# Kernel optimization log

Hardware: AMD Instinct MI355X
Metric: run time of the kernel (lower is better)

Reference implementation:

```python
import jax, jax.numpy as jnp
import numpy as np

N_NODES = 100000
N_EDGES = 3200000
IN_F, OUT_F = 256, 128


def setup_inputs() -> dict:
    key = jax.random.key(0)
    k1, k2, k3, k4, k5 = jax.random.split(key, 5)
    features = jax.random.normal(k1, (N_NODES, IN_F), dtype=jnp.float32)
    # Xavier-uniform-like init for the weight
    limit = float(np.sqrt(6.0 / (IN_F + OUT_F)))
    weight = jax.random.uniform(k2, (IN_F, OUT_F), dtype=jnp.float32, minval=-limit, maxval=limit)
    edge_row = jnp.sort(jax.random.randint(k3, (N_EDGES,), 0, N_NODES, dtype=jnp.int32))
    edge_col = jax.random.randint(k4, (N_EDGES,), 0, N_NODES, dtype=jnp.int32)
    edge_val = jax.random.uniform(k5, (N_EDGES,), dtype=jnp.float32)
    return {
        "features": features,
        "weight": weight,
        "edge_row": edge_row,
        "edge_col": edge_col,
        "edge_val": edge_val,
        "active": 1,
    }


def reference(features, weight, edge_row, edge_col, edge_val, active):
    # Dense transform: [N, in] @ [in, out] -> [N, out]
    h = features @ weight
    if active:  # static Python flag, matches `active=True` torch path
        h = jnp.tanh(h)
    # spmm(adj, h): out[r] = sum_e val[e] * h[col[e]] for edges with row[e]==r
    msgs = edge_val[:, None] * h[edge_col]          # [E, out] gather + scale
    out = jax.ops.segment_sum(msgs, edge_row, num_segments=N_NODES)
    return out
```

## Files before the change

kernel.cpp:

```cpp
#include <hip/hip_runtime.h>
#include <hip/hip_bf16.h>

#define N_NODES 100000
#define N_EDGES 3200000
#define IN_F 256
#define OUT_F 128

typedef __attribute__((ext_vector_type(8))) short bf16x8;
typedef __attribute__((ext_vector_type(4))) float f32x4;

__device__ __forceinline__ unsigned short f2bf(float f) {
    unsigned int u = __float_as_uint(f);
    u += 0x7fffu + ((u >> 16) & 1u);
    return (unsigned short)(u >> 16);
}

__device__ __forceinline__ short cvt_bf16(float f) {
    __hip_bfloat16 b = (__hip_bfloat16)f;
    return *reinterpret_cast<short*>(&b);
}

__global__ void k_init(const float* __restrict__ W, unsigned short* __restrict__ Wt,
                       const int* __restrict__ erow, int* __restrict__ row_ptr) {
    int e = blockIdx.x * 256 + threadIdx.x;
    if (e < IN_F * OUT_F) {
        int k = e >> 7;
        int c = e & 127;
        Wt[c * IN_F + k] = f2bf(W[e]);
    }
    if (e >= N_EDGES) return;
    int r = erow[e];
    int rprev = (e == 0) ? -1 : erow[e - 1];
    for (int rr = rprev + 1; rr <= r; ++rr) row_ptr[rr] = e;
    if (e == N_EDGES - 1) {
        for (int rr = r + 1; rr <= N_NODES; ++rr) row_ptr[rr] = N_EDGES;
    }
}

__global__ __launch_bounds__(256) void k_gemm(const float* __restrict__ A,
                                              const unsigned short* __restrict__ Wt,
                                              signed char* __restrict__ H8,
                                              const int* __restrict__ activep) {
    const int tid  = threadIdx.x;
    const int lane = tid & 63;
    const int wid  = tid >> 6;
    const int wr   = wid >> 1;
    const int wc   = wid & 1;
    const int brow = blockIdx.x * 128;
    const int l15  = lane & 15;
    const int lk   = (lane >> 4) * 8;

    const float* ap[4];
    #pragma unroll
    for (int i = 0; i < 4; ++i) {
        int row = brow + wr * 64 + i * 16 + l15;
        if (row > N_NODES - 1) row = N_NODES - 1;
        ap[i] = A + (long)row * IN_F + lk;
    }
    const unsigned short* bp = Wt + (long)(wc * 64 + l15) * IN_F + lk;

    f32x4 acc[4][4] = {};

    float4 f0[4], f1[4];
    #pragma unroll
    for (int i = 0; i < 4; ++i) {
        f0[i] = *(const float4*)(ap[i]);
        f1[i] = *(const float4*)(ap[i] + 4);
    }

    for (int k0 = 0; k0 < IN_F; k0 += 32) {
        const int kn = k0 + 32;
        float4 n0[4], n1[4];
        if (kn < IN_F) {
            #pragma unroll
            for (int i = 0; i < 4; ++i) {
                n0[i] = *(const float4*)(ap[i] + kn);
                n1[i] = *(const float4*)(ap[i] + kn + 4);
            }
        }
        bf16x8 a[4];
        #pragma unroll
        for (int i = 0; i < 4; ++i) {
            bf16x8 v;
            v[0] = cvt_bf16(f0[i].x); v[1] = cvt_bf16(f0[i].y);
            v[2] = cvt_bf16(f0[i].z); v[3] = cvt_bf16(f0[i].w);
            v[4] = cvt_bf16(f1[i].x); v[5] = cvt_bf16(f1[i].y);
            v[6] = cvt_bf16(f1[i].z); v[7] = cvt_bf16(f1[i].w);
            a[i] = v;
        }
        bf16x8 b[4];
        #pragma unroll
        for (int n = 0; n < 4; ++n)
            b[n] = *(const bf16x8*)(bp + (long)n * 16 * IN_F + k0);

        #pragma unroll
        for (int i = 0; i < 4; ++i)
            #pragma unroll
            for (int n = 0; n < 4; ++n)
                acc[i][n] = __builtin_amdgcn_mfma_f32_16x16x32_bf16(a[i], b[n], acc[i][n], 0, 0, 0);

        if (kn < IN_F) {
            #pragma unroll
            for (int i = 0; i < 4; ++i) { f0[i] = n0[i]; f1[i] = n1[i]; }
        }
    }

    const int act = *activep;
    const float qs = act ? 127.0f : 16.0f;
    #pragma unroll
    for (int i = 0; i < 4; ++i) {
        #pragma unroll
        for (int n = 0; n < 4; ++n) {
            #pragma unroll
            for (int r = 0; r < 4; ++r) {
                int row = brow + wr * 64 + i * 16 + (lane >> 4) * 4 + r;
                int col = wc * 64 + n * 16 + l15;
                if (row < N_NODES) {
                    float v = acc[i][n][r];
                    if (act) {
                        float t = __expf(2.0f * v);
                        v = 1.0f - __fdividef(2.0f, t + 1.0f);
                    }
                    float q = v * qs;
                    q = fminf(fmaxf(q, -127.0f), 127.0f);
                    H8[(long)row * OUT_F + col] = (signed char)__float2int_rn(q);
                }
            }
        }
    }
}

__global__ __launch_bounds__(256) void k_spmm(const int* __restrict__ row_ptr,
                                              const int* __restrict__ ecol,
                                              const float* __restrict__ eval,
                                              const signed char* __restrict__ h8,
                                              const int* __restrict__ activep,
                                              float* __restrict__ out) {
    const int lane = threadIdx.x & 63;
    const int w    = threadIdx.x >> 6;
    const int r    = blockIdx.x * 4 + w;
    if (r >= N_NODES) return;

    const int q  = lane >> 4;
    const int l15 = lane & 15;

    const int s = __builtin_amdgcn_readfirstlane(row_ptr[r]);
    const int e = __builtin_amdgcn_readfirstlane(row_ptr[r + 1]);
    const int act = __builtin_amdgcn_readfirstlane(*activep);
    const float invs = act ? (1.0f / 127.0f) : (1.0f / 16.0f);

    const signed char* hq = h8 + l15 * 8;

    float f0 = 0.f, f1 = 0.f, f2 = 0.f, f3 = 0.f;
    float f4 = 0.f, f5 = 0.f, f6 = 0.f, f7 = 0.f;

    for (int j = s; j < e; j += 16) {
        int   cc[4];
        float vv[4];
        #pragma unroll
        for (int u = 0; u < 4; ++u) {
            const int want = j + u * 4 + q;
            const int idx  = min(want, e - 1);
            cc[u] = ecol[idx];
            vv[u] = (want < e) ? eval[idx] * invs : 0.f;
        }
        uint2 g[4];
        #pragma unroll
        for (int u = 0; u < 4; ++u)
            g[u] = *(const uint2*)(hq + (((unsigned)cc[u]) << 7));
        #pragma unroll
        for (int u = 0; u < 4; ++u) {
            const float v = vv[u];
            const unsigned x = g[u].x, y = g[u].y;
            f0 = fmaf(v, (float)((signed char)(x      )), f0);
            f1 = fmaf(v, (float)((signed char)(x >>  8)), f1);
            f2 = fmaf(v, (float)((signed char)(x >> 16)), f2);
            f3 = fmaf(v, (float)((int)x >> 24),           f3);
            f4 = fmaf(v, (float)((signed char)(y      )), f4);
            f5 = fmaf(v, (float)((signed char)(y >>  8)), f5);
            f6 = fmaf(v, (float)((signed char)(y >> 16)), f6);
            f7 = fmaf(v, (float)((int)y >> 24),           f7);
        }
    }

    #pragma unroll
    for (int mask = 16; mask <= 32; mask <<= 1) {
        f0 += __shfl_xor(f0, mask);
        f1 += __shfl_xor(f1, mask);
        f2 += __shfl_xor(f2, mask);
        f3 += __shfl_xor(f3, mask);
        f4 += __shfl_xor(f4, mask);
        f5 += __shfl_xor(f5, mask);
        f6 += __shfl_xor(f6, mask);
        f7 += __shfl_xor(f7, mask);
    }

    if (q == 0) {
        float* dst = out + (long)r * OUT_F + l15 * 8;
        float4 o0; o0.x = f0; o0.y = f1; o0.z = f2; o0.w = f3;
        float4 o1; o1.x = f4; o1.y = f5; o1.z = f6; o1.w = f7;
        *(float4*)dst       = o0;
        *(float4*)(dst + 4) = o1;
    }
}

extern "C" void kernel_launch(void* const* d_in, const int* in_sizes, int n_in,
                              void* d_out, int out_size, void* d_ws, size_t ws_size,
                              hipStream_t stream) {
    const float* features = (const float*)d_in[0];
    const float* weight   = (const float*)d_in[1];
    const int*   erow     = (const int*)d_in[2];
    const int*   ecol     = (const int*)d_in[3];
    const float* evalp    = (const float*)d_in[4];
    const int*   activep  = (const int*)d_in[5];
    float* out = (float*)d_out;

    char* ws = (char*)d_ws;
    signed char* H8    = (signed char*)ws;
    unsigned short* Wt = (unsigned short*)(ws + 12800000);
    int* row_ptr       = (int*)(ws + 12800000 + 65536);

    k_init  <<<(N_EDGES + 255) / 256, 256, 0, stream>>>(weight, Wt, erow, row_ptr);
    k_gemm  <<<(N_NODES + 127) / 128, 256, 0, stream>>>(features, Wt, H8, activep);
    k_spmm  <<<(N_NODES + 3) / 4, 256, 0, stream>>>(row_ptr, ecol, evalp,
                                                    H8, activep, out);
}
```

Baseline: 149.3 us.

## Use biased uint8 features with hardware byte converts and deeper gather unroll in SpMM

The GEMM epilogue now stores the quantized features as unsigned bytes offset by 128. The SpMM converts them with v_cvt_f32_ubyteN and subtracts 128 times the sum of edge weights at the end, which removes the sign-extension shifts. The gather loop now processes 32 edges per iteration, with eight inline-asm dwordx2 loads using a scalar base and a 32-bit offset, followed by an explicit waitcnt. The goal is more memory-level parallelism and fewer ALU ops per edge. The cost is more registers, a forced full wait on each iteration, and extra float rounding from the bias subtraction.

Measured after the change: 158.7 us. 6.3% more time.

```diff
diff --git a/kernel.cpp b/kernel.cpp
--- a/kernel.cpp
+++ b/kernel.cpp
@@ -8,6 +8,7 @@
 
 typedef __attribute__((ext_vector_type(8))) short bf16x8;
 typedef __attribute__((ext_vector_type(4))) float f32x4;
+typedef __attribute__((ext_vector_type(2))) unsigned int u32x2;
 
 __device__ __forceinline__ unsigned short f2bf(float f) {
     unsigned int u = __float_as_uint(f);
@@ -19,6 +20,18 @@
     __hip_bfloat16 b = (__hip_bfloat16)f;
     return *reinterpret_cast<short*>(&b);
 }
+
+#if __has_builtin(__builtin_amdgcn_cvt_f32_ubyte0)
+#define UB0(x) __builtin_amdgcn_cvt_f32_ubyte0(x)
+#define UB1(x) __builtin_amdgcn_cvt_f32_ubyte1(x)
+#define UB2(x) __builtin_amdgcn_cvt_f32_ubyte2(x)
+#define UB3(x) __builtin_amdgcn_cvt_f32_ubyte3(x)
+#else
+#define UB0(x) ((float)((unsigned char)((x))))
+#define UB1(x) ((float)((unsigned char)((x) >> 8)))
+#define UB2(x) ((float)((unsigned char)((x) >> 16)))
+#define UB3(x) ((float)((x) >> 24))
+#endif
 
 __global__ void k_init(const float* __restrict__ W, unsigned short* __restrict__ Wt,
                        const int* __restrict__ erow, int* __restrict__ row_ptr) {
@@ -39,7 +52,7 @@
 
 __global__ __launch_bounds__(256) void k_gemm(const float* __restrict__ A,
                                               const unsigned short* __restrict__ Wt,
-                                              signed char* __restrict__ H8,
+                                              unsigned char* __restrict__ H8,
                                               const int* __restrict__ activep) {
     const int tid  = threadIdx.x;
     const int lane = tid & 63;
@@ -123,7 +136,8 @@
                     }
                     float q = v * qs;
                     q = fminf(fmaxf(q, -127.0f), 127.0f);
-                    H8[(long)row * OUT_F + col] = (signed char)__float2int_rn(q);
+                    H8[(long)row * OUT_F + col] =
+                        (unsigned char)(__float2int_rn(q) + 128);
                 }
             }
         }
@@ -133,7 +147,7 @@
 __global__ __launch_bounds__(256) void k_spmm(const int* __restrict__ row_ptr,
                                               const int* __restrict__ ecol,
                                               const float* __restrict__ eval,
-                                              const signed char* __restrict__ h8,
+                                              const unsigned char* __restrict__ h8,
                                               const int* __restrict__ activep,
                                               float* __restrict__ out) {
     const int lane = threadIdx.x & 63;
@@ -141,47 +155,72 @@
     const int r    = blockIdx.x * 4 + w;
     if (r >= N_NODES) return;
 
-    const int q  = lane >> 4;
+    const int q   = lane >> 4;
     const int l15 = lane & 15;
+    const unsigned dqb = (unsigned)l15 * 8u;
 
     const int s = __builtin_amdgcn_readfirstlane(row_ptr[r]);
     const int e = __builtin_amdgcn_readfirstlane(row_ptr[r + 1]);
     const int act = __builtin_amdgcn_readfirstlane(*activep);
     const float invs = act ? (1.0f / 127.0f) : (1.0f / 16.0f);
 
-    const signed char* hq = h8 + l15 * 8;
-
     float f0 = 0.f, f1 = 0.f, f2 = 0.f, f3 = 0.f;
     float f4 = 0.f, f5 = 0.f, f6 = 0.f, f7 = 0.f;
-
-    for (int j = s; j < e; j += 16) {
-        int   cc[4];
-        float vv[4];
-        #pragma unroll
-        for (int u = 0; u < 4; ++u) {
+    float vs = 0.f;
+
+    for (int j = s; j < e; j += 32) {
+        int   cc[8];
+        float vv[8];
+        #pragma unroll
+        for (int u = 0; u < 8; ++u) {
             const int want = j + u * 4 + q;
             const int idx  = min(want, e - 1);
             cc[u] = ecol[idx];
             vv[u] = (want < e) ? eval[idx] * invs : 0.f;
         }
-        uint2 g[4];
-        #pragma unroll
-        for (int u = 0; u < 4; ++u)
-            g[u] = *(const uint2*)(hq + (((unsigned)cc[u]) << 7));
-        #pragma unroll
-        for (int u = 0; u < 4; ++u) {
-            const float v = vv[u];
-            const unsigned x = g[u].x, y = g[u].y;
-            f0 = fmaf(v, (float)((signed char)(x      )), f0);
-            f1 = fmaf(v, (float)((signed char)(x >>  8)), f1);
-            f2 = fmaf(v, (float)((signed char)(x >> 16)), f2);
-            f3 = fmaf(v, (float)((int)x >> 24),           f3);
-            f4 = fmaf(v, (float)((signed char)(y      )), f4);
-            f5 = fmaf(v, (float)((signed char)(y >>  8)), f5);
-            f6 = fmaf(v, (float)((signed char)(y >> 16)), f6);
-            f7 = fmaf(v, (float)((int)y >> 24),           f7);
-        }
-    }
+        const unsigned o0 = dqb + (((unsigned)cc[0]) << 7);
+        const unsigned o1 = dqb + (((unsigned)cc[1]) << 7);
+        const unsigned o2 = dqb + (((unsigned)cc[2]) << 7);
+        const unsigned o3 = dqb + (((unsigned)cc[3]) << 7);
+        const unsigned o4 = dqb + (((unsigned)cc[4]) << 7);
+        const unsigned o5 = dqb + (((unsigned)cc[5]) << 7);
+        const unsigned o6 = dqb + (((unsigned)cc[6]) << 7);
+        const unsigned o7 = dqb + (((unsigned)cc[7]) << 7);
+
+        u32x2 g0, g1, g2, g3, g4, g5, g6, g7;
+        asm volatile("global_load_dwordx2 %0, %1, %2" : "=v"(g0) : "v"(o0), "s"(h8));
+        asm volatile("global_load_dwordx2 %0, %1, %2" : "=v"(g1) : "v"(o1), "s"(h8));
+        asm volatile("global_load_dwordx2 %0, %1, %2" : "=v"(g2) : "v"(o2), "s"(h8));
+        asm volatile("global_load_dwordx2 %0, %1, %2" : "=v"(g3) : "v"(o3), "s"(h8));
+        asm volatile("global_load_dwordx2 %0, %1, %2" : "=v"(g4) : "v"(o4), "s"(h8));
+        asm volatile("global_load_dwordx2 %0, %1, %2" : "=v"(g5) : "v"(o5), "s"(h8));
+        asm volatile("global_load_dwordx2 %0, %1, %2" : "=v"(g6) : "v"(o6), "s"(h8));
+        asm volatile("global_load_dwordx2 %0, %1, %2" : "=v"(g7) : "v"(o7), "s"(h8));
+        asm volatile("s_waitcnt vmcnt(0)" ::: "memory");
+        __builtin_amdgcn_sched_barrier(0);
+
+        #define EDGE_FMA(G, V)                      \
+            do {                                    \
+                const float v_ = (V);               \
+                vs += v_;                           \
+                const unsigned x_ = (G).x, y_ = (G).y; \
+                f0 = fmaf(v_, UB0(x_), f0);         \
+                f1 = fmaf(v_, UB1(x_), f1);         \
+                f2 = fmaf(v_, UB2(x_), f2);         \
+                f3 = fmaf(v_, UB3(x_), f3);         \
+                f4 = fmaf(v_, UB0(y_), f4);         \
+                f5 = fmaf(v_, UB1(y_), f5);         \
+                f6 = fmaf(v_, UB2(y_), f6);         \
+                f7 = fmaf(v_, UB3(y_), f7);         \
+            } while (0)
+        EDGE_FMA(g0, vv[0]); EDGE_FMA(g1, vv[1]); EDGE_FMA(g2, vv[2]); EDGE_FMA(g3, vv[3]);
+        EDGE_FMA(g4, vv[4]); EDGE_FMA(g5, vv[5]); EDGE_FMA(g6, vv[6]); EDGE_FMA(g7, vv[7]);
+        #undef EDGE_FMA
+    }
+
+    const float bias = 128.0f * vs;
+    f0 -= bias; f1 -= bias; f2 -= bias; f3 -= bias;
+    f4 -= bias; f5 -= bias; f6 -= bias; f7 -= bias;
 
     #pragma unroll
     for (int mask = 16; mask <= 32; mask <<= 1) {
@@ -197,10 +236,10 @@
 
     if (q == 0) {
         float* dst = out + (long)r * OUT_F + l15 * 8;
-        float4 o0; o0.x = f0; o0.y = f1; o0.z = f2; o0.w = f3;
-        float4 o1; o1.x = f4; o1.y = f5; o1.z = f6; o1.w = f7;
-        *(float4*)dst       = o0;
-        *(float4*)(dst + 4) = o1;
+        float4 o0v; o0v.x = f0; o0v.y = f1; o0v.z = f2; o0v.w = f3;
+        float4 o1v; o1v.x = f4; o1v.y = f5; o1v.z = f6; o1v.w = f7;
+        *(float4*)dst       = o0v;
+        *(float4*)(dst + 4) = o1v;
     }
 }
 
@@ -216,7 +255,7 @@
     float* out = (float*)d_out;
 
     char* ws = (char*)d_ws;
-    signed char* H8    = (signed char*)ws;
+    unsigned char* H8  = (unsigned char*)ws;
     unsigned short* Wt = (unsigned short*)(ws + 12800000);
     int* row_ptr       = (int*)(ws + 12800000 + 65536);
 
```

## Software-pipeline SpMM gathers and switch to offset-unsigned int8 encoding

Applied to the files above, without the earlier changes.

The SpMM loop is restructured into a two-stage software pipeline: edge indices and values are loaded two iterations ahead and the feature-row gathers one iteration ahead, so memory latency overlaps with the FMAs. The int8 features are stored biased by +128 as unsigned bytes, which allows cheaper unsigned byte-to-float conversion; the bias is removed afterwards using the sum of edge weights. Empty rows now take an early exit that writes zeros. The bias subtraction can add float rounding error, and the prefetch raises register pressure.

New measurement: 173.4 us. +16.2%, slower.

```diff
diff --git a/kernel.cpp b/kernel.cpp
--- a/kernel.cpp
+++ b/kernel.cpp
@@ -19,6 +19,11 @@
     __hip_bfloat16 b = (__hip_bfloat16)f;
     return *reinterpret_cast<short*>(&b);
 }
+
+#define UB0(x) ((float)((unsigned char)((x))))
+#define UB1(x) ((float)((unsigned char)((x) >> 8)))
+#define UB2(x) ((float)((unsigned char)((x) >> 16)))
+#define UB3(x) ((float)((x) >> 24))
 
 __global__ void k_init(const float* __restrict__ W, unsigned short* __restrict__ Wt,
                        const int* __restrict__ erow, int* __restrict__ row_ptr) {
@@ -39,7 +44,7 @@
 
 __global__ __launch_bounds__(256) void k_gemm(const float* __restrict__ A,
                                               const unsigned short* __restrict__ Wt,
-                                              signed char* __restrict__ H8,
+                                              unsigned char* __restrict__ H8,
                                               const int* __restrict__ activep) {
     const int tid  = threadIdx.x;
     const int lane = tid & 63;
@@ -123,7 +128,8 @@
                     }
                     float q = v * qs;
                     q = fminf(fmaxf(q, -127.0f), 127.0f);
-                    H8[(long)row * OUT_F + col] = (signed char)__float2int_rn(q);
+                    H8[(long)row * OUT_F + col] =
+                        (unsigned char)(__float2int_rn(q) + 128);
                 }
             }
         }
@@ -133,7 +139,7 @@
 __global__ __launch_bounds__(256) void k_spmm(const int* __restrict__ row_ptr,
                                               const int* __restrict__ ecol,
                                               const float* __restrict__ eval,
-                                              const signed char* __restrict__ h8,
+                                              const unsigned char* __restrict__ h8,
                                               const int* __restrict__ activep,
                                               float* __restrict__ out) {
     const int lane = threadIdx.x & 63;
@@ -141,47 +147,100 @@
     const int r    = blockIdx.x * 4 + w;
     if (r >= N_NODES) return;
 
-    const int q  = lane >> 4;
+    const int q   = lane >> 4;
     const int l15 = lane & 15;
+    const unsigned dqb = (unsigned)l15 * 8u;
 
     const int s = __builtin_amdgcn_readfirstlane(row_ptr[r]);
     const int e = __builtin_amdgcn_readfirstlane(row_ptr[r + 1]);
+
+    if (s >= e) {
+        if (q == 0) {
+            float4 z = {0.f, 0.f, 0.f, 0.f};
+            float* dst = out + (long)r * OUT_F + l15 * 8;
+            *(float4*)dst       = z;
+            *(float4*)(dst + 4) = z;
+        }
+        return;
+    }
+
     const int act = __builtin_amdgcn_readfirstlane(*activep);
     const float invs = act ? (1.0f / 127.0f) : (1.0f / 16.0f);
-
-    const signed char* hq = h8 + l15 * 8;
+    const unsigned char* hq = h8 + dqb;
 
     float f0 = 0.f, f1 = 0.f, f2 = 0.f, f3 = 0.f;
     float f4 = 0.f, f5 = 0.f, f6 = 0.f, f7 = 0.f;
+    float vs = 0.f;
+
+    #define LDE(jj, CC, VV)                                         \
+        do {                                                        \
+            _Pragma("unroll")                                       \
+            for (int u = 0; u < 4; ++u) {                           \
+                const int want = (jj) + u * 4 + q;                  \
+                const int idx  = min(want, e - 1);                  \
+                CC[u] = ecol[idx];                                  \
+                VV[u] = (want < e) ? eval[idx] * invs : 0.f;        \
+            }                                                       \
+        } while (0)
+
+    #define GATHER(CC, G)                                           \
+        do {                                                        \
+            _Pragma("unroll")                                       \
+            for (int u = 0; u < 4; ++u)                             \
+                G[u] = *(const uint2*)(hq + (((unsigned)CC[u]) << 7)); \
+        } while (0)
+
+    #define FMA8(G, V)                                              \
+        do {                                                        \
+            _Pragma("unroll")                                       \
+            for (int u = 0; u < 4; ++u) {                           \
+                const float v_ = V[u];                              \
+                vs += v_;                                           \
+                const unsigned x_ = G[u].x, y_ = G[u].y;            \
+                f0 = fmaf(v_, UB0(x_), f0);                         \
+                f1 = fmaf(v_, UB1(x_), f1);                         \
+                f2 = fmaf(v_, UB2(x_), f2);                         \
+                f3 = fmaf(v_, UB3(x_), f3);                         \
+                f4 = fmaf(v_, UB0(y_), f4);                         \
+                f5 = fmaf(v_, UB1(y_), f5);                         \
+                f6 = fmaf(v_, UB2(y_), f6);                         \
+                f7 = fmaf(v_, UB3(y_), f7);                         \
+            }                                                       \
+        } while (0)
+
+    int   ccB[4];
+    float vvA[4], vvB[4];
+    uint2 gA[4];
+    {
+        int ccA[4];
+        LDE(s, ccA, vvA);
+        GATHER(ccA, gA);
+        LDE(s + 16, ccB, vvB);
+    }
 
     for (int j = s; j < e; j += 16) {
-        int   cc[4];
-        float vv[4];
+        uint2 gB[4];
+        GATHER(ccB, gB);
+        int   ccN[4];
+        float vvN[4];
+        LDE(j + 32, ccN, vvN);
+        FMA8(gA, vvA);
         #pragma unroll
         for (int u = 0; u < 4; ++u) {
-            const int want = j + u * 4 + q;
-            const int idx  = min(want, e - 1);
-            cc[u] = ecol[idx];
-            vv[u] = (want < e) ? eval[idx] * invs : 0.f;
-        }
-        uint2 g[4];
-        #pragma unroll
-        for (int u = 0; u < 4; ++u)
-            g[u] = *(const uint2*)(hq + (((unsigned)cc[u]) << 7));
-        #pragma unroll
-        for (int u = 0; u < 4; ++u) {
-            const float v = vv[u];
-            const unsigned x = g[u].x, y = g[u].y;
-            f0 = fmaf(v, (float)((signed char)(x      )), f0);
-            f1 = fmaf(v, (float)((signed char)(x >>  8)), f1);
-            f2 = fmaf(v, (float)((signed char)(x >> 16)), f2);
-            f3 = fmaf(v, (float)((int)x >> 24),           f3);
-            f4 = fmaf(v, (float)((signed char)(y      )), f4);
-            f5 = fmaf(v, (float)((signed char)(y >>  8)), f5);
-            f6 = fmaf(v, (float)((signed char)(y >> 16)), f6);
-            f7 = fmaf(v, (float)((int)y >> 24),           f7);
-        }
-    }
+            gA[u]  = gB[u];
+            ccB[u] = ccN[u];
+            vvA[u] = vvB[u];
+            vvB[u] = vvN[u];
+        }
+    }
+
+    #undef LDE
+    #undef GATHER
+    #undef FMA8
+
+    const float bias = 128.0f * vs;
+    f0 -= bias; f1 -= bias; f2 -= bias; f3 -= bias;
+    f4 -= bias; f5 -= bias; f6 -= bias; f7 -= bias;
 
     #pragma unroll
     for (int mask = 16; mask <= 32; mask <<= 1) {
@@ -197,10 +256,10 @@
 
     if (q == 0) {
         float* dst = out + (long)r * OUT_F + l15 * 8;
-        float4 o0; o0.x = f0; o0.y = f1; o0.z = f2; o0.w = f3;
-        float4 o1; o1.x = f4; o1.y = f5; o1.z = f6; o1.w = f7;
-        *(float4*)dst       = o0;
-        *(float4*)(dst + 4) = o1;
+        float4 o0v; o0v.x = f0; o0v.y = f1; o0v.z = f2; o0v.w = f3;
+        float4 o1v; o1v.x = f4; o1v.y = f5; o1v.z = f6; o1v.w = f7;
+        *(float4*)dst       = o0v;
+        *(float4*)(dst + 4) = o1v;
     }
 }
 
@@ -216,7 +275,7 @@
     float* out = (float*)d_out;
 
     char* ws = (char*)d_ws;
-    signed char* H8    = (signed char*)ws;
+    unsigned char* H8  = (unsigned char*)ws;
     unsigned short* Wt = (unsigned short*)(ws + 12800000);
     int* row_ptr       = (int*)(ws + 12800000 + 65536);
 
```

## Switch SpMM to edge-chunk partitioning with atomic row flushes

Applied to the files above, without the earlier changes.

Drops the row_ptr construction and row-per-wavefront SpMM. Instead, each 16-lane group processes a fixed chunk of 104 consecutive edges, reading row, col and val with vector loads, and accumulates runs of equal rows before flushing them to the output with atomicAdd. H is stored as offset-unsigned bytes, corrected by subtracting 128 times the summed weights, which allows cheaper byte-to-float conversion. Costs added: a memset of the output, float atomics on the output, and non-deterministic summation order.

New measurement: 546.7 us. +266.2%, slower.

```diff
diff --git a/kernel.cpp b/kernel.cpp
--- a/kernel.cpp
+++ b/kernel.cpp
@@ -6,6 +6,9 @@
 #define IN_F 256
 #define OUT_F 128
 
+#define CHUNK 104
+#define SPMM_BLOCKS 1924
+
 typedef __attribute__((ext_vector_type(8))) short bf16x8;
 typedef __attribute__((ext_vector_type(4))) float f32x4;
 
@@ -20,26 +23,22 @@
     return *reinterpret_cast<short*>(&b);
 }
 
-__global__ void k_init(const float* __restrict__ W, unsigned short* __restrict__ Wt,
-                       const int* __restrict__ erow, int* __restrict__ row_ptr) {
-    int e = blockIdx.x * 256 + threadIdx.x;
-    if (e < IN_F * OUT_F) {
-        int k = e >> 7;
-        int c = e & 127;
-        Wt[c * IN_F + k] = f2bf(W[e]);
-    }
-    if (e >= N_EDGES) return;
-    int r = erow[e];
-    int rprev = (e == 0) ? -1 : erow[e - 1];
-    for (int rr = rprev + 1; rr <= r; ++rr) row_ptr[rr] = e;
-    if (e == N_EDGES - 1) {
-        for (int rr = r + 1; rr <= N_NODES; ++rr) row_ptr[rr] = N_EDGES;
-    }
+#define UB0(x) ((float)((unsigned char)((x))))
+#define UB1(x) ((float)((unsigned char)((x) >> 8)))
+#define UB2(x) ((float)((unsigned char)((x) >> 16)))
+#define UB3(x) ((float)((x) >> 24))
+
+__global__ void k_init(const float* __restrict__ W, unsigned short* __restrict__ Wt) {
+    int idx = blockIdx.x * 256 + threadIdx.x;
+    if (idx >= IN_F * OUT_F) return;
+    int k = idx >> 7;
+    int c = idx & 127;
+    Wt[c * IN_F + k] = f2bf(W[idx]);
 }
 
 __global__ __launch_bounds__(256) void k_gemm(const float* __restrict__ A,
                                               const unsigned short* __restrict__ Wt,
-                                              signed char* __restrict__ H8,
+                                              unsigned char* __restrict__ H8,
                                               const int* __restrict__ activep) {
     const int tid  = threadIdx.x;
     const int lane = tid & 63;
@@ -123,85 +122,106 @@
                     }
                     float q = v * qs;
                     q = fminf(fmaxf(q, -127.0f), 127.0f);
-                    H8[(long)row * OUT_F + col] = (signed char)__float2int_rn(q);
+                    H8[(long)row * OUT_F + col] =
+                        (unsigned char)(__float2int_rn(q) + 128);
                 }
             }
         }
     }
 }
 
-__global__ __launch_bounds__(256) void k_spmm(const int* __restrict__ row_ptr,
+__global__ __launch_bounds__(256) void k_spmm(const int* __restrict__ erow,
                                               const int* __restrict__ ecol,
                                               const float* __restrict__ eval,
-                                              const signed char* __restrict__ h8,
+                                              const unsigned char* __restrict__ h8,
                                               const int* __restrict__ activep,
                                               float* __restrict__ out) {
-    const int lane = threadIdx.x & 63;
-    const int w    = threadIdx.x >> 6;
-    const int r    = blockIdx.x * 4 + w;
-    if (r >= N_NODES) return;
-
-    const int q  = lane >> 4;
-    const int l15 = lane & 15;
-
-    const int s = __builtin_amdgcn_readfirstlane(row_ptr[r]);
-    const int e = __builtin_amdgcn_readfirstlane(row_ptr[r + 1]);
-    const int act = __builtin_amdgcn_readfirstlane(*activep);
+    const int tid  = threadIdx.x;
+    const int gid  = blockIdx.x * 16 + (tid >> 4);
+    const int l15  = tid & 15;
+    const int base = gid * CHUNK;
+    if (base >= N_EDGES) return;
+    const int end  = min(base + CHUNK, N_EDGES);
+
+    const int act = *activep;
     const float invs = act ? (1.0f / 127.0f) : (1.0f / 16.0f);
-
-    const signed char* hq = h8 + l15 * 8;
-
-    float f0 = 0.f, f1 = 0.f, f2 = 0.f, f3 = 0.f;
-    float f4 = 0.f, f5 = 0.f, f6 = 0.f, f7 = 0.f;
-
-    for (int j = s; j < e; j += 16) {
-        int   cc[4];
-        float vv[4];
-        #pragma unroll
-        for (int u = 0; u < 4; ++u) {
-            const int want = j + u * 4 + q;
-            const int idx  = min(want, e - 1);
-            cc[u] = ecol[idx];
-            vv[u] = (want < e) ? eval[idx] * invs : 0.f;
-        }
-        uint2 g[4];
-        #pragma unroll
-        for (int u = 0; u < 4; ++u)
-            g[u] = *(const uint2*)(hq + (((unsigned)cc[u]) << 7));
-        #pragma unroll
-        for (int u = 0; u < 4; ++u) {
-            const float v = vv[u];
-            const unsigned x = g[u].x, y = g[u].y;
-            f0 = fmaf(v, (float)((signed char)(x      )), f0);
-            f1 = fmaf(v, (float)((signed char)(x >>  8)), f1);
-            f2 = fmaf(v, (float)((signed char)(x >> 16)), f2);
-            f3 = fmaf(v, (float)((int)x >> 24),           f3);
-            f4 = fmaf(v, (float)((signed char)(y      )), f4);
-            f5 = fmaf(v, (float)((signed char)(y >>  8)), f5);
-            f6 = fmaf(v, (float)((signed char)(y >> 16)), f6);
-            f7 = fmaf(v, (float)((int)y >> 24),           f7);
-        }
-    }
-
-    #pragma unroll
-    for (int mask = 16; mask <= 32; mask <<= 1) {
-        f0 += __shfl_xor(f0, mask);
-        f1 += __shfl_xor(f1, mask);
-        f2 += __shfl_xor(f2, mask);
-        f3 += __shfl_xor(f3, mask);
-        f4 += __shfl_xor(f4, mask);
-        f5 += __shfl_xor(f5, mask);
-        f6 += __shfl_xor(f6, mask);
-        f7 += __shfl_xor(f7, mask);
-    }
-
-    if (q == 0) {
-        float* dst = out + (long)r * OUT_F + l15 * 8;
-        float4 o0; o0.x = f0; o0.y = f1; o0.z = f2; o0.w = f3;
-        float4 o1; o1.x = f4; o1.y = f5; o1.z = f6; o1.w = f7;
-        *(float4*)dst       = o0;
-        *(float4*)(dst + 4) = o1;
-    }
+    const unsigned char* hq  = h8 + l15 * 8;
+    float* const outq        = out + l15 * 8;
+
+    float a0 = 0.f, a1 = 0.f, a2 = 0.f, a3 = 0.f;
+    float a4 = 0.f, a5 = 0.f, a6 = 0.f, a7 = 0.f;
+    float vs = 0.f;
+    int cur = erow[base];
+
+    #define FLUSH(ROW)                                              \
+        do {                                                        \
+            float* dst_ = outq + (long)(ROW) * OUT_F;               \
+            const float b_ = 128.0f * vs;                           \
+            atomicAdd(dst_ + 0, a0 - b_);                           \
+            atomicAdd(dst_ + 1, a1 - b_);                           \
+            atomicAdd(dst_ + 2, a2 - b_);                           \
+            atomicAdd(dst_ + 3, a3 - b_);                           \
+            atomicAdd(dst_ + 4, a4 - b_);                           \
+            atomicAdd(dst_ + 5, a5 - b_);                           \
+            atomicAdd(dst_ + 6, a6 - b_);                           \
+            atomicAdd(dst_ + 7, a7 - b_);                           \
+            a0 = a1 = a2 = a3 = a4 = a5 = a6 = a7 = 0.f;            \
+            vs = 0.f;                                               \
+        } while (0)
+
+    #define ACC(T)                                                  \
+        do {                                                        \
+            const float v_ = vv[T];                                 \
+            vs += v_;                                               \
+            const unsigned x_ = g[T].x, y_ = g[T].y;                \
+            a0 = fmaf(v_, UB0(x_), a0);                             \
+            a1 = fmaf(v_, UB1(x_), a1);                             \
+            a2 = fmaf(v_, UB2(x_), a2);                             \
+            a3 = fmaf(v_, UB3(x_), a3);                             \
+            a4 = fmaf(v_, UB0(y_), a4);                             \
+            a5 = fmaf(v_, UB1(y_), a5);                             \
+            a6 = fmaf(v_, UB2(y_), a6);                             \
+            a7 = fmaf(v_, UB3(y_), a7);                             \
+        } while (0)
+
+    for (int b = base; b < end; b += 8) {
+        const int4   r0 = *(const int4*)(erow + b);
+        const int4   r1 = *(const int4*)(erow + b + 4);
+        const int4   c0 = *(const int4*)(ecol + b);
+        const int4   c1 = *(const int4*)(ecol + b + 4);
+        const float4 v0 = *(const float4*)(eval + b);
+        const float4 v1 = *(const float4*)(eval + b + 4);
+
+        uint2 g[8];
+        g[0] = *(const uint2*)(hq + (((unsigned)c0.x) << 7));
+        g[1] = *(const uint2*)(hq + (((unsigned)c0.y) << 7));
+        g[2] = *(const uint2*)(hq + (((unsigned)c0.z) << 7));
+        g[3] = *(const uint2*)(hq + (((unsigned)c0.w) << 7));
+        g[4] = *(const uint2*)(hq + (((unsigned)c1.x) << 7));
+        g[5] = *(const uint2*)(hq + (((unsigned)c1.y) << 7));
+        g[6] = *(const uint2*)(hq + (((unsigned)c1.z) << 7));
+        g[7] = *(const uint2*)(hq + (((unsigned)c1.w) << 7));
+
+        float vv[8];
+        vv[0] = v0.x * invs; vv[1] = v0.y * invs; vv[2] = v0.z * invs; vv[3] = v0.w * invs;
+        vv[4] = v1.x * invs; vv[5] = v1.y * invs; vv[6] = v1.z * invs; vv[7] = v1.w * invs;
+
+        if (r0.x == r1.w) {
+            if (r0.x != cur) { FLUSH(cur); cur = r0.x; }
+            ACC(0); ACC(1); ACC(2); ACC(3); ACC(4); ACC(5); ACC(6); ACC(7);
+        } else {
+            const int rr[8] = {r0.x, r0.y, r0.z, r0.w, r1.x, r1.y, r1.z, r1.w};
+            #pragma unroll
+            for (int t = 0; t < 8; ++t) {
+                if (rr[t] != cur) { FLUSH(cur); cur = rr[t]; }
+                ACC(t);
+            }
+        }
+    }
+    FLUSH(cur);
+
+    #undef FLUSH
+    #undef ACC
 }
 
 extern "C" void kernel_launch(void* const* d_in, const int* in_sizes, int n_in,
@@ -216,12 +236,11 @@
     float* out = (float*)d_out;
 
     char* ws = (char*)d_ws;
-    signed char* H8    = (signed char*)ws;
+    unsigned char* H8  = (unsigned char*)ws;
     unsigned short* Wt = (unsigned short*)(ws + 12800000);
-    int* row_ptr       = (int*)(ws + 12800000 + 65536);
-
-    k_init  <<<(N_EDGES + 255) / 256, 256, 0, stream>>>(weight, Wt, erow, row_ptr);
-    k_gemm  <<<(N_NODES + 127) / 128, 256, 0, stream>>>(features, Wt, H8, activep);
-    k_spmm  <<<(N_NODES + 3) / 4, 256, 0, stream>>>(row_ptr, ecol, evalp,
-                                                    H8, activep, out);
-}
+
+    hipMemsetAsync(out, 0, (size_t)out_size * sizeof(float), stream);
+    k_init <<<128, 256, 0, stream>>>(weight, Wt);
+    k_gemm <<<(N_NODES + 127) / 128, 256, 0, stream>>>(features, Wt, H8, activep);
+    k_spmm <<<SPMM_BLOCKS, 256, 0, stream>>>(erow, ecol, evalp, H8, activep, out);
+}
```
